# Kernel optimization log

Measured on AMD Instinct MI355X. Metric: run time of the kernel, lower is better.

## Reference

```python
import jax, jax.numpy as jnp
import numpy as np

N_BR, D, SD, RH, MH, UD, NOBS, B = 4, 256, 64, 64, 128, 16, 25, 32768
LN_EPS = 1e-5

def setup_inputs() -> dict:
    key = jax.random.key(0)
    ks = jax.random.split(key, 16)
    meas_in = D + SD
    rnn_in = RH + UD
    return {
        "z_dyn": jax.random.normal(ks[0], (B, D), jnp.float32),
        "z_static": jax.random.normal(ks[1], (B, SD), jnp.float32),
        "dt": jnp.ones((1,), jnp.float32),
        "ut": jax.random.normal(ks[2], (B, UD), jnp.float32),
        "gates": jax.random.normal(ks[3], (N_BR, D), jnp.float32) * 0.1,
        "W1": jax.random.normal(ks[4], (N_BR, MH, meas_in), jnp.float32) * (1.0 / np.sqrt(meas_in)),
        "b1": jnp.zeros((N_BR, MH), jnp.float32),
        "gamma": jnp.ones((N_BR, MH), jnp.float32),
        "beta": jnp.zeros((N_BR, MH), jnp.float32),
        "W2": jax.random.normal(ks[5], (N_BR, RH, MH), jnp.float32) * (1.0 / np.sqrt(MH)),
        "b2": jnp.zeros((N_BR, RH), jnp.float32),
        "lam_real": jnp.zeros((N_BR, RH), jnp.float32),
        "lam_imag": jax.random.normal(ks[6], (N_BR, RH), jnp.float32) * 0.1,
        "Bmat": jax.random.normal(ks[7], (N_BR, RH, rnn_in), jnp.float32) * (1.0 / np.sqrt(rnn_in)),
        "Wout": jax.random.normal(ks[8], (N_BR, D, RH), jnp.float32) * (1.0 / np.sqrt(RH)),
        "C": jax.random.normal(ks[9], (NOBS, D), jnp.float32) * (1.0 / np.sqrt(D)),
        "D": jax.random.normal(ks[10], (NOBS, UD), jnp.float32) * (1.0 / np.sqrt(UD)),
    }

def reference(z_dyn, z_static, dt, ut, gates, W1, b1, gamma, beta, W2, b2,
              lam_real, lam_imag, Bmat, Wout, C, D):
    ut_dt = ut * dt  # [B,u]
    n, Bsz = gates.shape[0], z_dyn.shape[0]
    # spectral gate per branch: [n,B,d]
    zg = z_dyn[None] * jax.nn.sigmoid(gates)[:, None, :]
    zs = jnp.broadcast_to(z_static[None], (n, Bsz, z_static.shape[-1]))
    x = jnp.concatenate([zg, zs], axis=-1)  # [n,B,meas_in]
    # measurement MLP: Linear -> LayerNorm -> GELU -> Linear
    h = jnp.einsum('nbi,nhi->nbh', x, W1) + b1[:, None, :]
    mu = h.mean(-1, keepdims=True)
    var = ((h - mu) ** 2).mean(-1, keepdims=True)
    h = (h - mu) / jnp.sqrt(var + LN_EPS) * gamma[:, None, :] + beta[:, None, :]
    h = jax.nn.gelu(h, approximate=False)
    g = jnp.einsum('nbh,noh->nbo', h, W2) + b2[:, None, :]  # [n,B,rnn_h]
    u_b = jnp.broadcast_to(ut_dt[None], (n, Bsz, ut_dt.shape[-1]))
    inp = jnp.concatenate([g, u_b], axis=-1)  # [n,B,rnn_h+u]
    b_inp = jnp.einsum('nbi,nhi->nbh', inp, Bmat)
    # complex recurrence step from h0 = 0 (as in forward())
    mag = jax.nn.sigmoid(lam_real) * 0.99
    lam_r = mag * jnp.cos(lam_imag)
    lam_i = mag * jnp.sin(lam_imag)
    h0r = jnp.zeros_like(b_inp)
    h0i = jnp.zeros_like(b_inp)
    h_real = h0r * lam_r[:, None, :] - h0i * lam_i[:, None, :] + b_inp
    # output projection per branch, summed over branches
    z_next = jnp.einsum('nbh,ndh->bd', h_real, Wout)
    yt = z_next @ C.T + ut_dt @ D.T
    return (z_next, yt)
```

## Files before the change

### kernel.cpp

```cpp
#include <hip/hip_runtime.h>
#include <hip/hip_bf16.h>

#define B_ROWS 32768
#define LN_EPS 1e-5f

typedef __bf16 bf16;
using bf16x8 = __attribute__((ext_vector_type(8))) __bf16;
using f32x4  = __attribute__((ext_vector_type(4))) float;


__device__ __forceinline__ float gelu_exact(float x) {
  float s = x * 0.70710678118f;
  float a = fabsf(s);
  float t = __builtin_amdgcn_rcpf(fmaf(0.3275911f, a, 1.0f));
  float p = fmaf(fmaf(fmaf(fmaf(1.061405429f, t, -1.453152027f),
                           t, 1.421413741f), t, -0.284496736f), t, 0.254829592f) * t;
  float e = __expf(-s * s);
  float er = fmaf(-p, e, 1.0f);
  er = copysignf(er, s);
  return 0.5f * x * (1.0f + er);
}

__global__ __launch_bounds__(256) void prep_weights1(
    const float* __restrict__ gates, const float* __restrict__ W1,
    const float* __restrict__ Bmat,  const float* __restrict__ W2,
    const float* __restrict__ b2,    const float* __restrict__ Wout,
    const float* __restrict__ Cm,
    bf16* __restrict__ W1sw, float* __restrict__ Mtmp, float* __restrict__ cvec,
    float* __restrict__ CW)
{
  const int stride = gridDim.x * blockDim.x;
  const int id = blockIdx.x * blockDim.x + threadIdx.x;
  for (int o = id; o < 512 * 320; o += stride) {
    int e = o & 7, m = (o >> 3) & 15, q2 = (o >> 7) & 3, rest = o >> 9;
    int kk = rest % 10, G = rest / 10;
    int n = G * 16 + m, k = kk * 32 + q2 * 8 + e;
    float wv = W1[n * 320 + k];
    if (k < 256) {
      float g = gates[(n >> 7) * 256 + k];
      wv *= 1.f / (1.f + __expf(-g));
    }
    W1sw[o] = (bf16)wv;
  }
  for (int i = id; i < 4 * 64 * 128; i += stride) {
    int n = i >> 13, r = (i >> 7) & 63, h = i & 127;
    float s = 0.f;
    for (int j = 0; j < 64; ++j)
      s += Bmat[(n * 64 + r) * 80 + j] * W2[(n * 64 + j) * 128 + h];
    Mtmp[i] = s;
  }
  for (int i = id; i < 256; i += stride) {
    int n = i >> 6, r = i & 63;
    float s = 0.f;
    for (int j = 0; j < 64; ++j)
      s += Bmat[(n * 64 + r) * 80 + j] * b2[n * 64 + j];
    cvec[i] = s;
  }
  for (int i = id; i < 25 * 256; i += stride) {
    int o = i >> 8, nr = i & 255;
    float s = 0.f;
    for (int d = 0; d < 256; ++d)
      s += Cm[o * 256 + d] * Wout[((nr >> 6) * 256 + d) * 64 + (nr & 63)];
    CW[i] = s;
  }
}

__global__ __launch_bounds__(256) void prep_weights2(
    const float* __restrict__ Wout, const float* __restrict__ Bmat,
    const float* __restrict__ Mtmp, const float* __restrict__ cvec,
    const float* __restrict__ CW,   const float* __restrict__ Dm,
    bf16* __restrict__ Psw)
{
  const int stride = gridDim.x * blockDim.x;
  const int id = blockIdx.x * blockDim.x + threadIdx.x;
  for (int o = id; o < 320 * 544; o += stride) {
    int e = o & 7, m = (o >> 3) & 15, q2 = (o >> 7) & 3, rest = o >> 9;
    int kk2 = rest % 17, G2 = rest / 17;
    int dd = G2 * 16 + m, cc = kk2 * 32 + q2 * 8 + e;
    float s = 0.f;
    if (dd < 281) {
      const bool isC = (dd >= 256);
      const int oo = dd - 256;
      if (cc < 512) {
        int n = cc >> 7, h = cc & 127;
        for (int r = 0; r < 64; ++r) {
          float wv = isC ? CW[(oo * 4 + n) * 64 + r] : Wout[(n * 256 + dd) * 64 + r];
          s += wv * Mtmp[(n * 64 + r) * 128 + h];
        }
      } else if (cc < 528) {
        int u = cc - 512;
        for (int n = 0; n < 4; ++n)
          for (int r = 0; r < 64; ++r) {
            float wv = isC ? CW[(oo * 4 + n) * 64 + r] : Wout[(n * 256 + dd) * 64 + r];
            s += wv * Bmat[(n * 64 + r) * 80 + 64 + u];
          }
        if (isC) s += Dm[oo * 16 + u];
      } else if (cc == 528) {
        for (int n = 0; n < 4; ++n)
          for (int r = 0; r < 64; ++r) {
            float wv = isC ? CW[(oo * 4 + n) * 64 + r] : Wout[(n * 256 + dd) * 64 + r];
            s += wv * cvec[n * 64 + r];
          }
      }
    }
    Psw[o] = (bf16)s;
  }
}

__global__ __launch_bounds__(256, 2) void fused_main(
    const float* __restrict__ zdyn, const float* __restrict__ zst,
    const float* __restrict__ ut,   const float* __restrict__ dtp,
    const bf16* __restrict__ W1sw,  const bf16* __restrict__ Psw,
    const float* __restrict__ b1,   const float* __restrict__ gamma,
    const float* __restrict__ beta,
    float* __restrict__ Z, float* __restrict__ yt)
{
  __shared__ __align__(16) bf16 Xs[64 * 320];
  __shared__ __align__(16) bf16 Hc[2 * 64 * 128];
  __shared__ __align__(16) bf16 Ht[64 * 32];
  __shared__ __align__(16) float partS[64 * 4];
  __shared__ __align__(16) float partQ[64 * 4];

  const int t = threadIdx.x;
  const int lane = t & 63, m16 = lane & 15, q = lane >> 4;
  const int w = t >> 6;
  const int rowBase = blockIdx.x * 64;

  #pragma unroll
  for (int a = 0; a < 10; ++a) {
    int g = a * 256 + t;
    int row = g / 40, pos = g - row * 40;
    int kk = pos >> 2, pq = pos & 3;
    int lq = pq ^ ((row >> 1) & 3);
    int col = kk * 32 + lq * 8;
    const float* src = (col < 256) ? &zdyn[(size_t)(rowBase + row) * 256 + col]
                                   : &zst[(size_t)(rowBase + row) * 64 + (col - 256)];
    float4 v0 = *(const float4*)src;
    float4 v1 = *(const float4*)(src + 4);
    bf16x8 o;
    o[0]=(bf16)v0.x; o[1]=(bf16)v0.y; o[2]=(bf16)v0.z; o[3]=(bf16)v0.w;
    o[4]=(bf16)v1.x; o[5]=(bf16)v1.y; o[6]=(bf16)v1.z; o[7]=(bf16)v1.w;
    *(bf16x8*)&Xs[(size_t)((kk * 64 + row) * 4 + pq) * 8] = o;
  }
  {
    const float dtv = dtp[0];
    int r = t >> 2, pq = t & 3;
    int lq = pq ^ ((r >> 1) & 3);
    bf16x8 o;
    #pragma unroll
    for (int e = 0; e < 8; ++e) {
      int ci = lq * 8 + e;
      float v = (ci < 16) ? ut[(size_t)(rowBase + r) * 16 + ci] * dtv
                          : (ci == 16 ? 1.f : 0.f);
      o[e] = (bf16)v;
    }
    *(bf16x8*)&Ht[t * 8] = o;
  }
  __syncthreads();

  f32x4 accZ[4][5];
  #pragma unroll
  for (int i = 0; i < 4; ++i)
    #pragma unroll
    for (int j = 0; j < 5; ++j)
      #pragma unroll
      for (int r = 0; r < 4; ++r) accZ[i][j][r] = 0.f;

  #pragma unroll 1
  for (int c = 0; c < 4; ++c) {
    const int hbuf = (c & 1) * 8192;

    float bbj[2], gmj[2], btj[2];
    #pragma unroll
    for (int j = 0; j < 2; ++j) {
      int col = c * 128 + w * 32 + j * 16 + m16;
      bbj[j] = b1[col]; gmj[j] = gamma[col]; btj[j] = beta[col];
    }

    f32x4 acc1[4][2];
    #pragma unroll
    for (int i = 0; i < 4; ++i)
      #pragma unroll
      for (int j = 0; j < 2; ++j)
        #pragma unroll
        for (int r = 0; r < 4; ++r) acc1[i][j][r] = 0.f;

    #pragma unroll
    for (int kk = 0; kk < 10; ++kk) {
      bf16x8 bfr[2];
      #pragma unroll
      for (int j = 0; j < 2; ++j) {
        int G = c * 8 + w * 2 + j;
        bfr[j] = *(const bf16x8*)&W1sw[(size_t)(((G * 10 + kk) * 4 + q) * 16 + m16) * 8];
      }
      bf16x8 af[4];
      #pragma unroll
      for (int i = 0; i < 4; ++i) {
        int row = i * 16 + m16;
        af[i] = *(const bf16x8*)&Xs[(size_t)((kk * 64 + row) * 4 + (q ^ ((row >> 1) & 3))) * 8];
      }
      __builtin_amdgcn_s_setprio(1);
      #pragma unroll
      for (int i = 0; i < 4; ++i)
        #pragma unroll
        for (int j = 0; j < 2; ++j)
          acc1[i][j] = __builtin_amdgcn_mfma_f32_16x16x32_bf16(af[i], bfr[j], acc1[i][j], 0, 0, 0);
      __builtin_amdgcn_s_setprio(0);
    }

    #pragma unroll
    for (int i = 0; i < 4; ++i)
      #pragma unroll
      for (int j = 0; j < 2; ++j)
        #pragma unroll
        for (int rr = 0; rr < 4; ++rr) acc1[i][j][rr] += bbj[j];

    #pragma unroll
    for (int i = 0; i < 4; ++i)
      #pragma unroll
      for (int rr = 0; rr < 4; ++rr) {
        float a0 = acc1[i][0][rr], a1 = acc1[i][1][rr];
        float s  = a0 + a1;
        float s2 = fmaf(a0, a0, a1 * a1);
        #pragma unroll
        for (int m = 1; m <= 8; m <<= 1) {
          s  += __shfl_xor(s,  m);
          s2 += __shfl_xor(s2, m);
        }
        if (m16 == 0) {
          int row = i * 16 + q * 4 + rr;
          partS[row * 4 + w] = s;
          partQ[row * 4 + w] = s2;
        }
      }
    __syncthreads();

    #pragma unroll
    for (int i = 0; i < 4; ++i) {
      #pragma unroll
      for (int rr = 0; rr < 4; ++rr) {
        int row = i * 16 + q * 4 + rr;
        f32x4 ps  = *(const f32x4*)&partS[row * 4];
        f32x4 pq2 = *(const f32x4*)&partQ[row * 4];
        float mu = (ps[0] + ps[1] + ps[2] + ps[3]) * 0.0078125f;
        float qq = (pq2[0] + pq2[1] + pq2[2] + pq2[3]) * 0.0078125f;
        float rs = rsqrtf(fmaxf(qq - mu * mu, 0.f) + LN_EPS);
        int rsw = (row >> 1) & 3;
        #pragma unroll
        for (int j = 0; j < 2; ++j) {
          float v = (acc1[i][j][rr] - mu) * rs;
          v = fmaf(v, gmj[j], btj[j]);
          int lq2 = (j * 2 + (m16 >> 3)) ^ rsw;
          Hc[hbuf + ((w * 64 + row) * 4 + lq2) * 8 + (m16 & 7)] = (bf16)gelu_exact(v);
        }
      }
    }
    __syncthreads();

    #pragma unroll
    for (int tk = 0; tk < 4; ++tk) {
      int kk2 = c * 4 + tk;
      bf16x8 af[4], bfr[5];
      #pragma unroll
      for (int i = 0; i < 4; ++i) {
        int row = i * 16 + m16;
        af[i] = *(const bf16x8*)&Hc[hbuf + ((tk * 64 + row) * 4 + (q ^ ((row >> 1) & 3))) * 8];
      }
      #pragma unroll
      for (int j = 0; j < 5; ++j) {
        int G2 = w * 5 + j;
        bfr[j] = *(const bf16x8*)&Psw[(size_t)(((G2 * 17 + kk2) * 4 + q) * 16 + m16) * 8];
      }
      __builtin_amdgcn_s_setprio(1);
      #pragma unroll
      for (int i = 0; i < 4; ++i)
        #pragma unroll
        for (int j = 0; j < 5; ++j)
          accZ[i][j] = __builtin_amdgcn_mfma_f32_16x16x32_bf16(af[i], bfr[j], accZ[i][j], 0, 0, 0);
      __builtin_amdgcn_s_setprio(0);
    }
  }

  {
    bf16x8 af[4], bfr[5];
    #pragma unroll
    for (int i = 0; i < 4; ++i) {
      int row = i * 16 + m16;
      af[i] = *(const bf16x8*)&Ht[(row * 4 + (q ^ ((row >> 1) & 3))) * 8];
    }
    #pragma unroll
    for (int j = 0; j < 5; ++j) {
      int G2 = w * 5 + j;
      bfr[j] = *(const bf16x8*)&Psw[(size_t)(((G2 * 17 + 16) * 4 + q) * 16 + m16) * 8];
    }
    __builtin_amdgcn_s_setprio(1);
    #pragma unroll
    for (int i = 0; i < 4; ++i)
      #pragma unroll
      for (int j = 0; j < 5; ++j)
        accZ[i][j] = __builtin_amdgcn_mfma_f32_16x16x32_bf16(af[i], bfr[j], accZ[i][j], 0, 0, 0);
    __builtin_amdgcn_s_setprio(0);
  }

  #pragma unroll
  for (int i = 0; i < 4; ++i)
    #pragma unroll
    for (int j = 0; j < 5; ++j) {
      int col = w * 80 + j * 16 + m16;
      #pragma unroll
      for (int rr = 0; rr < 4; ++rr) {
        int row = rowBase + i * 16 + q * 4 + rr;
        if (col < 256) Z[(size_t)row * 256 + col] = accZ[i][j][rr];
        else if (col < 281) yt[(size_t)row * 25 + (col - 256)] = accZ[i][j][rr];
      }
    }
}

extern "C" void kernel_launch(void* const* d_in, const int* in_sizes, int n_in,
                              void* d_out, int out_size, void* d_ws, size_t ws_size,
                              hipStream_t stream) {
  const float* zdyn  = (const float*)d_in[0];
  const float* zst   = (const float*)d_in[1];
  const float* dtp   = (const float*)d_in[2];
  const float* ut    = (const float*)d_in[3];
  const float* gates = (const float*)d_in[4];
  const float* W1    = (const float*)d_in[5];
  const float* b1    = (const float*)d_in[6];
  const float* gamma = (const float*)d_in[7];
  const float* beta  = (const float*)d_in[8];
  const float* W2    = (const float*)d_in[9];
  const float* b2    = (const float*)d_in[10];
  const float* Bmat  = (const float*)d_in[13];
  const float* Wout  = (const float*)d_in[14];
  const float* Cm    = (const float*)d_in[15];
  const float* Dm    = (const float*)d_in[16];

  char* ws = (char*)d_ws;
  bf16*  W1sw = (bf16*)(ws);
  bf16*  Psw  = (bf16*)(ws + 327680);
  float* Mtmp = (float*)(ws + 675840);
  float* cvec = (float*)(ws + 806912);
  float* CW   = (float*)(ws + 807936);

  float* Z  = (float*)d_out;
  float* yt = Z + (size_t)B_ROWS * 256;

  hipLaunchKernelGGL(prep_weights1, dim3(256), dim3(256), 0, stream,
                     gates, W1, Bmat, W2, b2, Wout, Cm, W1sw, Mtmp, cvec, CW);
  hipLaunchKernelGGL(prep_weights2, dim3(512), dim3(256), 0, stream,
                     Wout, Bmat, Mtmp, cvec, CW, Dm, Psw);
  hipLaunchKernelGGL(fused_main, dim3(512), dim3(256), 0, stream,
                     zdyn, zst, ut, dtp, W1sw, Psw, b1, gamma, beta, Z, yt);
}
```

Baseline: 215.8 us.

## Split fused_main rows across 8 waves with 512-thread blocks

Doubles the block to 512 threads (8 waves) and arranges the waves 2x4, so each wave handles 32 rows instead of 64. This halves per-wave accumulator state, cutting register pressure, and launch bounds now target 4 blocks per CU for more latency hiding. The cost is that each B-fragment of the weights is loaded from global/L2 by twice as many waves, and block-wide syncs coordinate more waves.

```diff
diff --git a/kernel.cpp b/kernel.cpp
--- a/kernel.cpp
+++ b/kernel.cpp
@@ -107,7 +107,7 @@
   }
 }
 
-__global__ __launch_bounds__(256, 2) void fused_main(
+__global__ __launch_bounds__(512, 4) void fused_main(
     const float* __restrict__ zdyn, const float* __restrict__ zst,
     const float* __restrict__ ut,   const float* __restrict__ dtp,
     const bf16* __restrict__ W1sw,  const bf16* __restrict__ Psw,
@@ -124,11 +124,13 @@
   const int t = threadIdx.x;
   const int lane = t & 63, m16 = lane & 15, q = lane >> 4;
   const int w = t >> 6;
+  const int wr = w >> 2;
+  const int wc = w & 3;
   const int rowBase = blockIdx.x * 64;
 
   #pragma unroll
-  for (int a = 0; a < 10; ++a) {
-    int g = a * 256 + t;
+  for (int a = 0; a < 5; ++a) {
+    int g = a * 512 + t;
     int row = g / 40, pos = g - row * 40;
     int kk = pos >> 2, pq = pos & 3;
     int lq = pq ^ ((row >> 1) & 3);
@@ -142,7 +144,7 @@
     o[4]=(bf16)v1.x; o[5]=(bf16)v1.y; o[6]=(bf16)v1.z; o[7]=(bf16)v1.w;
     *(bf16x8*)&Xs[(size_t)((kk * 64 + row) * 4 + pq) * 8] = o;
   }
-  {
+  if (t < 256) {
     const float dtv = dtp[0];
     int r = t >> 2, pq = t & 3;
     int lq = pq ^ ((r >> 1) & 3);
@@ -158,9 +160,9 @@
   }
   __syncthreads();
 
-  f32x4 accZ[4][5];
+  f32x4 accZ[2][5];
   #pragma unroll
-  for (int i = 0; i < 4; ++i)
+  for (int i = 0; i < 2; ++i)
     #pragma unroll
     for (int j = 0; j < 5; ++j)
       #pragma unroll
@@ -173,13 +175,13 @@
     float bbj[2], gmj[2], btj[2];
     #pragma unroll
     for (int j = 0; j < 2; ++j) {
-      int col = c * 128 + w * 32 + j * 16 + m16;
+      int col = c * 128 + wc * 32 + j * 16 + m16;
       bbj[j] = b1[col]; gmj[j] = gamma[col]; btj[j] = beta[col];
     }
 
-    f32x4 acc1[4][2];
-    #pragma unroll
-    for (int i = 0; i < 4; ++i)
+    f32x4 acc1[2][2];
+    #pragma unroll
+    for (int i = 0; i < 2; ++i)
       #pragma unroll
       for (int j = 0; j < 2; ++j)
         #pragma unroll
@@ -190,18 +192,18 @@
       bf16x8 bfr[2];
       #pragma unroll
       for (int j = 0; j < 2; ++j) {
-        int G = c * 8 + w * 2 + j;
+        int G = c * 8 + wc * 2 + j;
         bfr[j] = *(const bf16x8*)&W1sw[(size_t)(((G * 10 + kk) * 4 + q) * 16 + m16) * 8];
       }
-      bf16x8 af[4];
-      #pragma unroll
-      for (int i = 0; i < 4; ++i) {
-        int row = i * 16 + m16;
+      bf16x8 af[2];
+      #pragma unroll
+      for (int i = 0; i < 2; ++i) {
+        int row = wr * 32 + i * 16 + m16;
         af[i] = *(const bf16x8*)&Xs[(size_t)((kk * 64 + row) * 4 + (q ^ ((row >> 1) & 3))) * 8];
       }
       __builtin_amdgcn_s_setprio(1);
       #pragma unroll
-      for (int i = 0; i < 4; ++i)
+      for (int i = 0; i < 2; ++i)
         #pragma unroll
         for (int j = 0; j < 2; ++j)
           acc1[i][j] = __builtin_amdgcn_mfma_f32_16x16x32_bf16(af[i], bfr[j], acc1[i][j], 0, 0, 0);
@@ -209,14 +211,14 @@
     }
 
     #pragma unroll
-    for (int i = 0; i < 4; ++i)
+    for (int i = 0; i < 2; ++i)
       #pragma unroll
       for (int j = 0; j < 2; ++j)
         #pragma unroll
         for (int rr = 0; rr < 4; ++rr) acc1[i][j][rr] += bbj[j];
 
     #pragma unroll
-    for (int i = 0; i < 4; ++i)
+    for (int i = 0; i < 2; ++i)
       #pragma unroll
       for (int rr = 0; rr < 4; ++rr) {
         float a0 = acc1[i][0][rr], a1 = acc1[i][1][rr];
@@ -228,18 +230,18 @@
           s2 += __shfl_xor(s2, m);
         }
         if (m16 == 0) {
-          int row = i * 16 + q * 4 + rr;
-          partS[row * 4 + w] = s;
-          partQ[row * 4 + w] = s2;
+          int row = wr * 32 + i * 16 + q * 4 + rr;
+          partS[row * 4 + wc] = s;
+          partQ[row * 4 + wc] = s2;
         }
       }
     __syncthreads();
 
     #pragma unroll
-    for (int i = 0; i < 4; ++i) {
+    for (int i = 0; i < 2; ++i) {
       #pragma unroll
       for (int rr = 0; rr < 4; ++rr) {
-        int row = i * 16 + q * 4 + rr;
+        int row = wr * 32 + i * 16 + q * 4 + rr;
         f32x4 ps  = *(const f32x4*)&partS[row * 4];
         f32x4 pq2 = *(const f32x4*)&partQ[row * 4];
         float mu = (ps[0] + ps[1] + ps[2] + ps[3]) * 0.0078125f;
@@ -251,7 +253,7 @@
           float v = (acc1[i][j][rr] - mu) * rs;
           v = fmaf(v, gmj[j], btj[j]);
           int lq2 = (j * 2 + (m16 >> 3)) ^ rsw;
-          Hc[hbuf + ((w * 64 + row) * 4 + lq2) * 8 + (m16 & 7)] = (bf16)gelu_exact(v);
+          Hc[hbuf + ((wc * 64 + row) * 4 + lq2) * 8 + (m16 & 7)] = (bf16)gelu_exact(v);
         }
       }
     }
@@ -260,20 +262,20 @@
     #pragma unroll
     for (int tk = 0; tk < 4; ++tk) {
       int kk2 = c * 4 + tk;
-      bf16x8 af[4], bfr[5];
-      #pragma unroll
-      for (int i = 0; i < 4; ++i) {
-        int row = i * 16 + m16;
+      bf16x8 af[2], bfr[5];
+      #pragma unroll
+      for (int i = 0; i < 2; ++i) {
+        int row = wr * 32 + i * 16 + m16;
         af[i] = *(const bf16x8*)&Hc[hbuf + ((tk * 64 + row) * 4 + (q ^ ((row >> 1) & 3))) * 8];
       }
       #pragma unroll
       for (int j = 0; j < 5; ++j) {
-        int G2 = w * 5 + j;
+        int G2 = wc * 5 + j;
         bfr[j] = *(const bf16x8*)&Psw[(size_t)(((G2 * 17 + kk2) * 4 + q) * 16 + m16) * 8];
       }
       __builtin_amdgcn_s_setprio(1);
       #pragma unroll
-      for (int i = 0; i < 4; ++i)
+      for (int i = 0; i < 2; ++i)
         #pragma unroll
         for (int j = 0; j < 5; ++j)
           accZ[i][j] = __builtin_amdgcn_mfma_f32_16x16x32_bf16(af[i], bfr[j], accZ[i][j], 0, 0, 0);
@@ -282,20 +284,20 @@
   }
 
   {
-    bf16x8 af[4], bfr[5];
-    #pragma unroll
-    for (int i = 0; i < 4; ++i) {
-      int row = i * 16 + m16;
+    bf16x8 af[2], bfr[5];
+    #pragma unroll
+    for (int i = 0; i < 2; ++i) {
+      int row = wr * 32 + i * 16 + m16;
       af[i] = *(const bf16x8*)&Ht[(row * 4 + (q ^ ((row >> 1) & 3))) * 8];
     }
     #pragma unroll
     for (int j = 0; j < 5; ++j) {
-      int G2 = w * 5 + j;
+      int G2 = wc * 5 + j;
       bfr[j] = *(const bf16x8*)&Psw[(size_t)(((G2 * 17 + 16) * 4 + q) * 16 + m16) * 8];
     }
     __builtin_amdgcn_s_setprio(1);
     #pragma unroll
-    for (int i = 0; i < 4; ++i)
+    for (int i = 0; i < 2; ++i)
       #pragma unroll
       for (int j = 0; j < 5; ++j)
         accZ[i][j] = __builtin_amdgcn_mfma_f32_16x16x32_bf16(af[i], bfr[j], accZ[i][j], 0, 0, 0);
@@ -303,13 +305,13 @@
   }
 
   #pragma unroll
-  for (int i = 0; i < 4; ++i)
+  for (int i = 0; i < 2; ++i)
     #pragma unroll
     for (int j = 0; j < 5; ++j) {
-      int col = w * 80 + j * 16 + m16;
+      int col = wc * 80 + j * 16 + m16;
       #pragma unroll
       for (int rr = 0; rr < 4; ++rr) {
-        int row = rowBase + i * 16 + q * 4 + rr;
+        int row = rowBase + wr * 32 + i * 16 + q * 4 + rr;
         if (col < 256) Z[(size_t)row * 256 + col] = accZ[i][j][rr];
         else if (col < 281) yt[(size_t)row * 25 + (col - 256)] = accZ[i][j][rr];
       }
@@ -349,6 +351,6 @@
                      gates, W1, Bmat, W2, b2, Wout, Cm, W1sw, Mtmp, cvec, CW);
   hipLaunchKernelGGL(prep_weights2, dim3(512), dim3(256), 0, stream,
                      Wout, Bmat, Mtmp, cvec, CW, Dm, Psw);
-  hipLaunchKernelGGL(fused_main, dim3(512), dim3(256), 0, stream,
+  hipLaunchKernelGGL(fused_main, dim3(512), dim3(512), 0, stream,
                      zdyn, zst, ut, dtp, W1sw, Psw, b1, gamma, beta, Z, yt);
 }
```

After: 245.5 us. +13.8%, slower.
